# Performance work log

Measured on AMD Instinct MI355X. Metric: run time of the kernel, lower is better.

Reference implementation:

```python
import jax, jax.numpy as jnp
import numpy as np

N1 = 50000
N2 = 50000
NN = 16
NI = 64
ND = 128


def setup_inputs() -> dict:
    key = jax.random.key(0)
    ks = jax.random.split(key, 12)
    inp = {
        "features1": jax.random.normal(ks[0], (N1, NI), dtype=jnp.float32),
        "features2": jax.random.normal(ks[1], (N2, NI), dtype=jnp.float32),
        "x1": jax.random.normal(ks[2], (N1, 3), dtype=jnp.float32),
        "x2": jax.random.normal(ks[3], (N2, 3), dtype=jnp.float32),
        "nuv1": jax.random.normal(ks[4], (N1, 3, 3), dtype=jnp.float32),
        "nuv2": jax.random.normal(ks[5], (N2, 3, 3), dtype=jnp.float32),
        "topk": jax.random.randint(ks[6], (N1, NN), 0, N2, dtype=jnp.int64),
        # query_f params: Linear(2*Ni, Nd) -> ELU -> Linear(Nd, Nd) -> ELU
        "W1": jax.random.normal(ks[7], (2 * NI, ND), dtype=jnp.float32) * (1.0 / np.sqrt(2 * NI)),
        "b1": jnp.zeros((ND,), dtype=jnp.float32),
        "W2": jax.random.normal(ks[8], (ND, ND), dtype=jnp.float32) * (1.0 / np.sqrt(ND)),
        "b2": jnp.zeros((ND,), dtype=jnp.float32),
        "radius": jnp.float32(1.0),
    }
    return inp


def reference(features1, features2, x1, x2, nuv1, nuv2, topk, W1, b1, W2, b2, radius):
    # gather neighbor features: [N1, nn, Ni]
    feats_nn = features2[topk]
    # concat with self features broadcast over neighbor axis: [N1, nn, 2*Ni]
    feat_self = jnp.broadcast_to(features1[:, None, :], feats_nn.shape)
    h = jnp.concatenate([feats_nn, feat_self], axis=-1)
    # small fused MLP (query_f)
    h = jax.nn.elu(h @ W1 + b1)
    h = jax.nn.elu(h @ W2 + b2)  # [N1, nn, Nd]
    # distance-weighted aggregation
    x_nn = x2[topk]                          # [N1, nn, 3]
    orient = x_nn - x1[:, None, :]
    dis2 = jnp.sum(orient * orient, axis=2)  # [N1, nn]
    w = jnp.exp(-dis2 / (2.0 * radius * radius))
    w = jnp.where(topk == 0, jnp.float32(0.0), w)  # mask padded (index-0) neighbors
    # weighted matmul reduction: [N1, Nd]
    out = jnp.einsum("nk,nkd->nd", w, h)
    return out
```

## Files before the change

### kernel.cpp

```cpp
#include <hip/hip_runtime.h>

#define N1C 50000
#define N2C 50000
#define NNC 16
#define NIC 64
#define NDC 128
#define QB  16
#define MR  256
#define FELEMS (N1C * NIC)

typedef __bf16 bf16x8 __attribute__((ext_vector_type(8)));
typedef float f32x4 __attribute__((ext_vector_type(4)));
typedef unsigned u32x4 __attribute__((ext_vector_type(4)));

#if defined(__has_builtin)
#if __has_builtin(__builtin_amdgcn_cvt_pk_bf16_f32)
#define HAVE_PK_BF16 1
#endif
#endif

#ifdef HAVE_PK_BF16
typedef __bf16 bf16x2 __attribute__((ext_vector_type(2)));
static __device__ __forceinline__ unsigned int pkbf(float a, float b) {
    bf16x2 r = __builtin_amdgcn_cvt_pk_bf16_f32(a, b);
    return __builtin_bit_cast(unsigned int, r);
}
#else
static __device__ __forceinline__ unsigned short f2bf_sw(float f) {
    unsigned int u = __builtin_bit_cast(unsigned int, f);
    u += 0x7fffu + ((u >> 16) & 1u);
    return (unsigned short)(u >> 16);
}
static __device__ __forceinline__ unsigned int pkbf(float a, float b) {
    return (unsigned int)f2bf_sw(a) | ((unsigned int)f2bf_sw(b) << 16);
}
#endif

static __device__ __forceinline__ float elu(float x) {
    return x > 0.f ? x : __expf(x) - 1.f;
}

static __device__ __forceinline__ void stage16(const uint4* gsrc_lane, uint4* ldst_base) {
#if defined(__has_builtin) && __has_builtin(__builtin_amdgcn_global_load_lds)
    __builtin_amdgcn_global_load_lds(
        (const __attribute__((address_space(1))) void*)gsrc_lane,
        (__attribute__((address_space(3))) void*)ldst_base, 16, 0, 0);
#else
    ldst_base[threadIdx.x & 63] = *gsrc_lane;
#endif
}

__global__ void prep_w(const float* __restrict__ W1, const float* __restrict__ W2,
                       unsigned short* __restrict__ wsW) {
    const int idx  = blockIdx.x * 256 + threadIdx.x;
    const int m    = idx >> 14;
    const int o    = idx & 16383;
    const int j    = o & 7;
    const int lane = (o >> 3) & 63;
    const int ksmt = o >> 9;
    const int ks   = ksmt & 3;
    const int mt   = ksmt >> 2;
    const int d = mt * 16 + (lane & 15);
    const int k = ks * 32 + (lane >> 4) * 8 + j;
    const float* W = m ? W2 : W1;
    wsW[idx] = (unsigned short)pkbf(W[(size_t)k * NDC + d], 0.f);
}

__global__ void prep_f(const float* __restrict__ f1, const float* __restrict__ f2,
                       unsigned short* __restrict__ dst) {
    const int g = blockIdx.x * 256 + threadIdx.x;
    const size_t base = (size_t)g * 8;
    const float* src = (base < FELEMS) ? (f1 + base) : (f2 + base - FELEMS);
    const float4 v0 = *(const float4*)src;
    const float4 v1 = *(const float4*)(src + 4);
    uint4 o;
    o.x = pkbf(v0.x, v0.y);
    o.y = pkbf(v0.z, v0.w);
    o.z = pkbf(v1.x, v1.y);
    o.w = pkbf(v1.z, v1.w);
    *(uint4*)(dst + base) = o;
}

__global__ __launch_bounds__(512, 4)
void fused_knn_mlp(const unsigned short* __restrict__ f1b,
                   const unsigned short* __restrict__ f2b,
                   const float* __restrict__ x1,
                   const float* __restrict__ x2,
                   const int*   __restrict__ topk,
                   const float* __restrict__ b1,
                   const float* __restrict__ b2,
                   const float* __restrict__ radius,
                   const unsigned short* __restrict__ wsW,
                   float* __restrict__ out)
{
    __shared__ uint4 sW[4096];

    const int tid  = threadIdx.x;
    const int blk  = blockIdx.x;
    const int lane = tid & 63;
    const int wave = tid >> 6;
    const int quad = lane >> 4;
    const int l16  = lane & 15;
    const int rloc = wave * 32 + l16;

    const uint4* wp = (const uint4*)wsW;

    #pragma unroll
    for (int it = 0; it < 8; ++it) {
        const int base = wave * 512 + it * 64;
        stage16(wp + base + lane, sW + base);
    }

    const int idx0 = topk[blk * MR + rloc];
    const int idx1 = topk[blk * MR + rloc + 16];
    const int q0   = blk * QB + wave * 2;
    const int q1   = q0 + 1;

    uint4 xf0[4], xf1[4];
    #pragma unroll
    for (int ks = 0; ks < 2; ++ks) {
        xf0[ks] = *(const uint4*)(f2b + (size_t)idx0 * NIC + ks * 32 + quad * 8);
        xf1[ks] = *(const uint4*)(f2b + (size_t)idx1 * NIC + ks * 32 + quad * 8);
        xf0[ks + 2] = *(const uint4*)(f1b + (size_t)q0 * NIC + ks * 32 + quad * 8);
        xf1[ks + 2] = *(const uint4*)(f1b + (size_t)q1 * NIC + ks * 32 + quad * 8);
    }

    float wg0, wg1;
    {
        const float rr = radius[0];
        const float inv2r2 = 1.f / (2.f * rr * rr);
        const float dx0 = x2[idx0 * 3 + 0] - x1[q0 * 3 + 0];
        const float dy0 = x2[idx0 * 3 + 1] - x1[q0 * 3 + 1];
        const float dz0 = x2[idx0 * 3 + 2] - x1[q0 * 3 + 2];
        const float dx1 = x2[idx1 * 3 + 0] - x1[q1 * 3 + 0];
        const float dy1 = x2[idx1 * 3 + 1] - x1[q1 * 3 + 1];
        const float dz1 = x2[idx1 * 3 + 2] - x1[q1 * 3 + 2];
        wg0 = (idx0 == 0) ? 0.f : __expf(-(dx0 * dx0 + dy0 * dy0 + dz0 * dz0) * inv2r2);
        wg1 = (idx1 == 0) ? 0.f : __expf(-(dx1 * dx1 + dy1 * dy1 + dz1 * dz1) * inv2r2);
    }

    __syncthreads();

    unsigned P[8][2][2];
    #pragma unroll
    for (int mp = 0; mp < 4; ++mp) {
        f32x4 accp[2][2];
        #pragma unroll
        for (int mi = 0; mi < 2; ++mi) {
            accp[mi][0] = (f32x4){0.f, 0.f, 0.f, 0.f};
            accp[mi][1] = accp[mi][0];
        }
        #pragma unroll
        for (int ks = 0; ks < 4; ++ks) {
            const bf16x8 x0  = __builtin_bit_cast(bf16x8, xf0[ks]);
            const bf16x8 x1v = __builtin_bit_cast(bf16x8, xf1[ks]);
            #pragma unroll
            for (int mi = 0; mi < 2; ++mi) {
                const int mt = mp * 2 + mi;
                const bf16x8 a = *(const bf16x8*)&sW[(mt * 4 + ks) * 64 + lane];
                accp[mi][0] = __builtin_amdgcn_mfma_f32_16x16x32_bf16(a, x0,  accp[mi][0], 0, 0, 0);
                accp[mi][1] = __builtin_amdgcn_mfma_f32_16x16x32_bf16(a, x1v, accp[mi][1], 0, 0, 0);
            }
        }
        #pragma unroll
        for (int mi = 0; mi < 2; ++mi) {
            const int mt = mp * 2 + mi;
            const float4 b1v = *(const float4*)(b1 + mt * 16 + quad * 4);
            #pragma unroll
            for (int nt = 0; nt < 2; ++nt) {
                P[mt][nt][0] = pkbf(elu(accp[mi][nt][0] + b1v.x), elu(accp[mi][nt][1] + b1v.y));
                P[mt][nt][1] = pkbf(elu(accp[mi][nt][2] + b1v.z), elu(accp[mi][nt][3] + b1v.w));
            }
        }
    }

    f32x4 acc2[2][8];
    #pragma unroll
    for (int nt2 = 0; nt2 < 8; ++nt2) {
        acc2[0][nt2] = (f32x4){0.f, 0.f, 0.f, 0.f};
        acc2[1][nt2] = acc2[0][nt2];
    }
    #pragma unroll
    for (int ks = 0; ks < 4; ++ks) {
        u32x4 a2[2];
        #pragma unroll
        for (int mt2 = 0; mt2 < 2; ++mt2) {
            #pragma unroll
            for (int u = 0; u < 4; ++u) {
                const int src = (((quad * 2) + (u >> 1)) & 3) * 16 + l16;
                const unsigned lo = __shfl(P[2 * ks][mt2][u & 1], src, 64);
                const unsigned hi = __shfl(P[2 * ks + 1][mt2][u & 1], src, 64);
                a2[mt2][u] = (quad & 2) ? hi : lo;
            }
        }
        const bf16x8 af0 = __builtin_bit_cast(bf16x8, a2[0]);
        const bf16x8 af1 = __builtin_bit_cast(bf16x8, a2[1]);
        #pragma unroll
        for (int nt2 = 0; nt2 < 8; ++nt2) {
            const bf16x8 b = *(const bf16x8*)&sW[2048 + (nt2 * 4 + ks) * 64 + lane];
            acc2[0][nt2] = __builtin_amdgcn_mfma_f32_16x16x32_bf16(af0, b, acc2[0][nt2], 0, 0, 0);
            acc2[1][nt2] = __builtin_amdgcn_mfma_f32_16x16x32_bf16(af1, b, acc2[1][nt2], 0, 0, 0);
        }
    }

    float wk0[4], wk1[4];
    #pragma unroll
    for (int reg = 0; reg < 4; ++reg) {
        const int src = (lane & 48) | (quad * 4 + reg);
        wk0[reg] = __shfl(wg0, src, 64);
        wk1[reg] = __shfl(wg1, src, 64);
    }
    #pragma unroll
    for (int mt2 = 0; mt2 < 2; ++mt2) {
        #pragma unroll
        for (int nt2 = 0; nt2 < 8; ++nt2) {
            const int d2 = nt2 * 16 + l16;
            const float bb = b2[d2];
            float s;
            if (mt2 == 0)
                s = elu(acc2[0][nt2][0] + bb) * wk0[0] + elu(acc2[0][nt2][1] + bb) * wk0[1]
                  + elu(acc2[0][nt2][2] + bb) * wk0[2] + elu(acc2[0][nt2][3] + bb) * wk0[3];
            else
                s = elu(acc2[1][nt2][0] + bb) * wk1[0] + elu(acc2[1][nt2][1] + bb) * wk1[1]
                  + elu(acc2[1][nt2][2] + bb) * wk1[2] + elu(acc2[1][nt2][3] + bb) * wk1[3];
            s += __shfl_xor(s, 16, 64);
            s += __shfl_xor(s, 32, 64);
            if (lane < 16) {
                out[(size_t)(blk * QB + wave * 2 + mt2) * NDC + d2] = s;
            }
        }
    }
}

extern "C" void kernel_launch(void* const* d_in, const int* in_sizes, int n_in,
                              void* d_out, int out_size, void* d_ws, size_t ws_size,
                              hipStream_t stream) {
    const float* features1 = (const float*)d_in[0];
    const float* features2 = (const float*)d_in[1];
    const float* x1        = (const float*)d_in[2];
    const float* x2        = (const float*)d_in[3];
    const int*   topk      = (const int*)d_in[6];
    const float* W1        = (const float*)d_in[7];
    const float* b1        = (const float*)d_in[8];
    const float* W2        = (const float*)d_in[9];
    const float* b2        = (const float*)d_in[10];
    const float* radius    = (const float*)d_in[11];
    float* out = (float*)d_out;

    unsigned short* wsW = (unsigned short*)d_ws;
    unsigned short* f1b = wsW + 32768;
    unsigned short* f2b = f1b + FELEMS;

    prep_w<<<dim3(128), 256, 0, stream>>>(W1, W2, wsW);
    prep_f<<<dim3(3125), 256, 0, stream>>>(features1, features2, f1b);
    fused_knn_mlp<<<dim3(N1C / QB), 512, 0, stream>>>(f1b, f2b, x1, x2, topk,
                                                      b1, b2, radius, wsW, out);
}
```

Measured before the change: 201.0 us.

## Merge prep kernels, fold biases into MFMA accumulators, use permlane32 swap

Merges the two preprocessing kernels into one launch by splitting work on block index, which removes one kernel launch. Initializes the MFMA accumulators with b1 and b2 so the per-element bias adds in the ELU epilogues go away. Replaces the four-shuffle transpose of layer-1 outputs with a permlane32_swap plus one xor shuffle when the builtin is available, reducing cross-lane traffic. The new lane-exchange path depends on getting the quad mapping exactly right and only runs when the compiler exposes the builtin.

```diff
diff --git a/kernel.cpp b/kernel.cpp
--- a/kernel.cpp
+++ b/kernel.cpp
@@ -17,6 +17,9 @@
 #if __has_builtin(__builtin_amdgcn_cvt_pk_bf16_f32)
 #define HAVE_PK_BF16 1
 #endif
+#if __has_builtin(__builtin_amdgcn_permlane32_swap)
+#define HAVE_PL32 1
+#endif
 #endif
 
 #ifdef HAVE_PK_BF16
@@ -50,35 +53,37 @@
 #endif
 }
 
-__global__ void prep_w(const float* __restrict__ W1, const float* __restrict__ W2,
-                       unsigned short* __restrict__ wsW) {
-    const int idx  = blockIdx.x * 256 + threadIdx.x;
-    const int m    = idx >> 14;
-    const int o    = idx & 16383;
-    const int j    = o & 7;
-    const int lane = (o >> 3) & 63;
-    const int ksmt = o >> 9;
-    const int ks   = ksmt & 3;
-    const int mt   = ksmt >> 2;
-    const int d = mt * 16 + (lane & 15);
-    const int k = ks * 32 + (lane >> 4) * 8 + j;
-    const float* W = m ? W2 : W1;
-    wsW[idx] = (unsigned short)pkbf(W[(size_t)k * NDC + d], 0.f);
-}
-
-__global__ void prep_f(const float* __restrict__ f1, const float* __restrict__ f2,
-                       unsigned short* __restrict__ dst) {
-    const int g = blockIdx.x * 256 + threadIdx.x;
-    const size_t base = (size_t)g * 8;
-    const float* src = (base < FELEMS) ? (f1 + base) : (f2 + base - FELEMS);
-    const float4 v0 = *(const float4*)src;
-    const float4 v1 = *(const float4*)(src + 4);
-    uint4 o;
-    o.x = pkbf(v0.x, v0.y);
-    o.y = pkbf(v0.z, v0.w);
-    o.z = pkbf(v1.x, v1.y);
-    o.w = pkbf(v1.z, v1.w);
-    *(uint4*)(dst + base) = o;
+__global__ void prep_all(const float* __restrict__ f1, const float* __restrict__ f2,
+                         const float* __restrict__ W1, const float* __restrict__ W2,
+                         unsigned short* __restrict__ fdst,
+                         unsigned short* __restrict__ wsW) {
+    const int blk = blockIdx.x;
+    if (blk < 3125) {
+        const int g = blk * 256 + threadIdx.x;
+        const size_t base = (size_t)g * 8;
+        const float* src = (base < FELEMS) ? (f1 + base) : (f2 + base - FELEMS);
+        const float4 v0 = *(const float4*)src;
+        const float4 v1 = *(const float4*)(src + 4);
+        uint4 o;
+        o.x = pkbf(v0.x, v0.y);
+        o.y = pkbf(v0.z, v0.w);
+        o.z = pkbf(v1.x, v1.y);
+        o.w = pkbf(v1.z, v1.w);
+        *(uint4*)(fdst + base) = o;
+    } else {
+        const int idx  = (blk - 3125) * 256 + threadIdx.x;
+        const int m    = idx >> 14;
+        const int o    = idx & 16383;
+        const int j    = o & 7;
+        const int lane = (o >> 3) & 63;
+        const int ksmt = o >> 9;
+        const int ks   = ksmt & 3;
+        const int mt   = ksmt >> 2;
+        const int d = mt * 16 + (lane & 15);
+        const int k = ks * 32 + (lane >> 4) * 8 + j;
+        const float* W = m ? W2 : W1;
+        wsW[idx] = (unsigned short)pkbf(W[(size_t)k * NDC + d], 0.f);
+    }
 }
 
 __global__ __launch_bounds__(512, 4)
@@ -147,7 +152,8 @@
         f32x4 accp[2][2];
         #pragma unroll
         for (int mi = 0; mi < 2; ++mi) {
-            accp[mi][0] = (f32x4){0.f, 0.f, 0.f, 0.f};
+            const float4 b1v = *(const float4*)(b1 + (mp * 2 + mi) * 16 + quad * 4);
+            accp[mi][0] = (f32x4){b1v.x, b1v.y, b1v.z, b1v.w};
             accp[mi][1] = accp[mi][0];
         }
         #pragma unroll
@@ -165,11 +171,10 @@
         #pragma unroll
         for (int mi = 0; mi < 2; ++mi) {
             const int mt = mp * 2 + mi;
-            const float4 b1v = *(const float4*)(b1 + mt * 16 + quad * 4);
             #pragma unroll
             for (int nt = 0; nt < 2; ++nt) {
-                P[mt][nt][0] = pkbf(elu(accp[mi][nt][0] + b1v.x), elu(accp[mi][nt][1] + b1v.y));
-                P[mt][nt][1] = pkbf(elu(accp[mi][nt][2] + b1v.z), elu(accp[mi][nt][3] + b1v.w));
+                P[mt][nt][0] = pkbf(elu(accp[mi][nt][0]), elu(accp[mi][nt][1]));
+                P[mt][nt][1] = pkbf(elu(accp[mi][nt][2]), elu(accp[mi][nt][3]));
             }
         }
     }
@@ -177,14 +182,28 @@
     f32x4 acc2[2][8];
     #pragma unroll
     for (int nt2 = 0; nt2 < 8; ++nt2) {
-        acc2[0][nt2] = (f32x4){0.f, 0.f, 0.f, 0.f};
+        const float bb = b2[nt2 * 16 + l16];
+        acc2[0][nt2] = (f32x4){bb, bb, bb, bb};
         acc2[1][nt2] = acc2[0][nt2];
     }
+    const bool qodd = (quad & 1) != 0;
     #pragma unroll
     for (int ks = 0; ks < 4; ++ks) {
         u32x4 a2[2];
         #pragma unroll
         for (int mt2 = 0; mt2 < 2; ++mt2) {
+#ifdef HAVE_PL32
+            #pragma unroll
+            for (int e = 0; e < 2; ++e) {
+                auto pr = __builtin_amdgcn_permlane32_swap(
+                    P[2 * ks][mt2][e], P[2 * ks + 1][mt2][e], false, false);
+                const unsigned Rv = qodd ? (unsigned)pr[1] : (unsigned)pr[0];
+                const unsigned Zv = qodd ? (unsigned)pr[0] : (unsigned)pr[1];
+                const unsigned Sv = __shfl_xor(Zv, 16, 64);
+                a2[mt2][e]     = qodd ? Sv : Rv;
+                a2[mt2][2 + e] = qodd ? Rv : Sv;
+            }
+#else
             #pragma unroll
             for (int u = 0; u < 4; ++u) {
                 const int src = (((quad * 2) + (u >> 1)) & 3) * 16 + l16;
@@ -192,6 +211,7 @@
                 const unsigned hi = __shfl(P[2 * ks + 1][mt2][u & 1], src, 64);
                 a2[mt2][u] = (quad & 2) ? hi : lo;
             }
+#endif
         }
         const bf16x8 af0 = __builtin_bit_cast(bf16x8, a2[0]);
         const bf16x8 af1 = __builtin_bit_cast(bf16x8, a2[1]);
@@ -215,14 +235,13 @@
         #pragma unroll
         for (int nt2 = 0; nt2 < 8; ++nt2) {
             const int d2 = nt2 * 16 + l16;
-            const float bb = b2[d2];
             float s;
             if (mt2 == 0)
-                s = elu(acc2[0][nt2][0] + bb) * wk0[0] + elu(acc2[0][nt2][1] + bb) * wk0[1]
-                  + elu(acc2[0][nt2][2] + bb) * wk0[2] + elu(acc2[0][nt2][3] + bb) * wk0[3];
+                s = elu(acc2[0][nt2][0]) * wk0[0] + elu(acc2[0][nt2][1]) * wk0[1]
+                  + elu(acc2[0][nt2][2]) * wk0[2] + elu(acc2[0][nt2][3]) * wk0[3];
             else
-                s = elu(acc2[1][nt2][0] + bb) * wk1[0] + elu(acc2[1][nt2][1] + bb) * wk1[1]
-                  + elu(acc2[1][nt2][2] + bb) * wk1[2] + elu(acc2[1][nt2][3] + bb) * wk1[3];
+                s = elu(acc2[1][nt2][0]) * wk1[0] + elu(acc2[1][nt2][1]) * wk1[1]
+                  + elu(acc2[1][nt2][2]) * wk1[2] + elu(acc2[1][nt2][3]) * wk1[3];
             s += __shfl_xor(s, 16, 64);
             s += __shfl_xor(s, 32, 64);
             if (lane < 16) {
@@ -251,8 +270,7 @@
     unsigned short* f1b = wsW + 32768;
     unsigned short* f2b = f1b + FELEMS;
 
-    prep_w<<<dim3(128), 256, 0, stream>>>(W1, W2, wsW);
-    prep_f<<<dim3(3125), 256, 0, stream>>>(features1, features2, f1b);
+    prep_all<<<dim3(3253), 256, 0, stream>>>(features1, features2, W1, W2, f1b, wsW);
     fused_knn_mlp<<<dim3(N1C / QB), 512, 0, stream>>>(f1b, f2b, x1, x2, topk,
                                                       b1, b2, radius, wsW, out);
 }
```

After: 187.1 us. 6.9% less time.
